# Optimization experiments

Hardware: AMD Instinct MI355X
Metric: run time of the kernel (lower is better)

The kernel has to match this reference:

```python
import jax, jax.numpy as jnp
import numpy as np

UNITS = 1024
EMBED = 512
K = 32000
HIDDEN_LAYERS = 2
BATCH = 64
SEQ = 256
ALPHA = 0.2  # leaky_relu slope


def _leaky_relu(z):
    return jnp.where(z > 0, z, ALPHA * z)


def setup_inputs() -> dict:
    key = jax.random.key(0)
    ks = jax.random.split(key, 10)
    s_in = 1.0 / np.sqrt(UNITS)
    s_e = 1.0 / np.sqrt(EMBED)
    return {
        "x": jax.random.randint(ks[0], (BATCH, SEQ), 0, K),
        "x_embedding": jax.random.normal(ks[1], (K, EMBED), dtype=jnp.float32) * 0.05,
        "w_y": jax.random.normal(ks[2], (UNITS, UNITS), dtype=jnp.float32) * s_in,
        "w_x": jax.random.normal(ks[3], (EMBED, UNITS), dtype=jnp.float32) * s_e,
        "b_in": jax.random.uniform(ks[4], (UNITS,), dtype=jnp.float32, minval=-0.05, maxval=0.05),
        "w_hidden": jax.random.normal(ks[5], (HIDDEN_LAYERS, UNITS, UNITS), dtype=jnp.float32) * s_in,
        "b_hidden": jax.random.uniform(ks[6], (HIDDEN_LAYERS, UNITS), dtype=jnp.float32, minval=-0.05, maxval=0.05),
        "w_out": jax.random.normal(ks[7], (UNITS, UNITS), dtype=jnp.float32) * s_in,
        "b_out": jax.random.uniform(ks[8], (UNITS,), dtype=jnp.float32, minval=-0.05, maxval=0.05),
        "h0": jax.random.uniform(ks[9], (1, UNITS), dtype=jnp.float32, minval=-0.05, maxval=0.05),
    }


def reference(x, x_embedding, w_y, w_x, b_in, w_hidden, b_hidden, w_out, b_out, h0):
    n = x.shape[0]
    # Gather all embeddings up front: [n, T, E] -> time-major [T, n, E]
    xe_all = jnp.swapaxes(x_embedding[x], 0, 1)

    def step(y0, xe):
        # MLPUnit: sum of input projections + bias, inner activation
        h = _leaky_relu(y0 @ w_y + xe @ w_x + b_in)

        def layer(hc, wb):
            w, bb = wb
            return _leaky_relu(hc @ w + bb), None

        h, _ = jax.lax.scan(layer, h, (w_hidden, b_hidden))
        y1 = y0 + (h @ w_out + b_out)  # highway residual
        return y1, y1

    y0 = jnp.broadcast_to(h0, (n, h0.shape[1]))
    _, yr = jax.lax.scan(step, y0, xe_all)  # [T, n, units]
    return jnp.swapaxes(yr, 0, 1)  # [n, T, units]
```

## Files before the change

### kernel.cpp

```cpp
#include <hip/hip_runtime.h>


constexpr int B = 64, T = 256, U = 1024, E = 512;
constexpr int BU = B * U;
constexpr int APITCH = 1156;
constexpr int RPITCH = 264;

#define LRELU(v) ((v) > 0.f ? (v) : 0.2f * (v))

using f4 = float __attribute__((ext_vector_type(4)));

__device__ __forceinline__ void llc_store(float* p, float v) {
  __hip_atomic_store(p, v, __ATOMIC_RELAXED, __HIP_MEMORY_SCOPE_AGENT);
}
__device__ __forceinline__ unsigned llc_flag(const unsigned* p) {
  return __hip_atomic_load(p, __ATOMIC_RELAXED, __HIP_MEMORY_SCOPE_AGENT);
}
__device__ __forceinline__ void llc_post(unsigned* p, unsigned v) {
  __hip_atomic_store(p, v, __ATOMIC_RELAXED, __HIP_MEMORY_SCOPE_AGENT);
}

__global__ void k_init(float* __restrict__ slot1, float* __restrict__ ybuf,
                       const float* __restrict__ h0,
                       unsigned* __restrict__ flags) {
  int tid = blockIdx.x * 256 + threadIdx.x;
  if (tid < 512) flags[tid] = 0u;
  if (tid < BU) {
    float v = h0[tid & (U - 1)];
    slot1[tid] = v;
    ybuf[tid] = v;
  }
}

__global__ __launch_bounds__(256) void k_xproj(
    const int* __restrict__ x, const float* __restrict__ emb,
    const float* __restrict__ w_x, const float* __restrict__ b_in,
    float* __restrict__ xp) {
  __shared__ float a_s[64][36];
  __shared__ float w_s[32][64];
  __shared__ int idxs[64];
  const int tid = threadIdx.x;
  const int m0 = blockIdx.x * 64;
  const int c0 = blockIdx.y * 64;
  if (tid < 64) {
    int m = m0 + tid;
    idxs[tid] = x[(m & 63) * T + (m >> 6)];
  }
  __syncthreads();
  const int rq = tid >> 4, cq = tid & 15;
  float acc[4][4] = {};
  for (int k0 = 0; k0 < E; k0 += 32) {
#pragma unroll
    for (int rep = 0; rep < 8; ++rep) {
      int e = rep * 256 + tid;
      int r = e >> 5, k = e & 31;
      a_s[r][k] = emb[(size_t)idxs[r] * E + k0 + k];
    }
#pragma unroll
    for (int rep = 0; rep < 2; ++rep) {
      int e = rep * 256 + tid;
      int kr = e >> 4, q = e & 15;
      *(float4*)&w_s[kr][4 * q] =
          *(const float4*)(w_x + (size_t)(k0 + kr) * U + c0 + 4 * q);
    }
    __syncthreads();
#pragma unroll
    for (int kc = 0; kc < 32; kc += 4) {
      float4 a4[4], w4[4];
#pragma unroll
      for (int i = 0; i < 4; ++i) a4[i] = *(const float4*)&a_s[4 * rq + i][kc];
#pragma unroll
      for (int kk = 0; kk < 4; ++kk)
        w4[kk] = *(const float4*)&w_s[kc + kk][4 * cq];
#pragma unroll
      for (int i = 0; i < 4; ++i) {
        const float av[4] = {a4[i].x, a4[i].y, a4[i].z, a4[i].w};
#pragma unroll
        for (int kk = 0; kk < 4; ++kk) {
          acc[i][0] += av[kk] * w4[kk].x;
          acc[i][1] += av[kk] * w4[kk].y;
          acc[i][2] += av[kk] * w4[kk].z;
          acc[i][3] += av[kk] * w4[kk].w;
        }
      }
    }
    __syncthreads();
  }
  const float4 bb = *(const float4*)(b_in + c0 + 4 * cq);
  const float bv[4] = {bb.x, bb.y, bb.z, bb.w};
#pragma unroll
  for (int i = 0; i < 4; ++i) {
    float4 o;
    o.x = acc[i][0] + bv[0];
    o.y = acc[i][1] + bv[1];
    o.z = acc[i][2] + bv[2];
    o.w = acc[i][3] + bv[3];
    *(float4*)(xp + (size_t)(m0 + 4 * rq + i) * U + c0 + 4 * cq) = o;
  }
}

__global__ __launch_bounds__(512, 2) void k_seq(
    const float* __restrict__ xp, const float* __restrict__ w_y,
    const float* __restrict__ w_h, const float* __restrict__ b_h,
    const float* __restrict__ w_out, const float* __restrict__ b_out,
    float* __restrict__ out, float* __restrict__ slots,
    float* __restrict__ ybuf, unsigned* __restrict__ flags) {
  __shared__ float a_s[8 * APITCH];
  __shared__ float red2[64 * RPITCH];
  const int tid = threadIdx.x;
  const int bid = blockIdx.x;
  const int cg = ((bid & 7) << 2) | ((bid >> 3) & 3);
  const int rg = bid >> 5;
  const int w = tid >> 6, l = tid & 63;
  const int ci = l & 7;
  const int sp = w * 8 + (l >> 3);
  const int cb = 4 * ci, k0 = 16 * sp;
  const int abase_k = 36 * (sp >> 1) + 16 * (sp & 1);
  const int frow = 8 * rg + (tid >> 5);
  const int fu = 32 * cg + (tid & 31);
  const int tb = tid >> 8;
  const int kq = ((tid & 255) + 8 * cg) & 255;
  const int lofs = 36 * (kq >> 3) + ((4 * kq) & 31);

  auto wbase = [&](int P) -> const float* {
    const int p = P & 3;
    const float* Wsrc = (p == 0)   ? w_y
                        : (p == 3) ? w_out
                                   : w_h + (size_t)(p - 1) * U * U;
    return Wsrc + (size_t)k0 * U + 32 * cg + cb;
  };
  f4 wreg[16];
  {
    const float* wp = wbase(0);
#pragma unroll
    for (int j = 0; j < 16; ++j) wreg[j] = *(const f4*)(wp + (size_t)j * U);
  }

  for (int P = 0; P < 4 * T; ++P) {
    const int t = P >> 2, p = P & 3;
    const float* Asrc =
        slots + (size_t)((P + 1) & 1) * BU + (size_t)(8 * rg) * U;
    float* slotw = slots + (size_t)(P & 1) * BU;
    if (P > 0) {
      if (tid < 64) {
        const unsigned tgt = (unsigned)P;
        const unsigned* fp = &flags[rg * 32 + (l & 31)];
        while (!__all(llc_flag(fp) >= tgt)) __builtin_amdgcn_s_sleep(1);
      }
      __syncthreads();
      asm volatile("" ::: "memory");
    }
    float preA = 0.f, preB = 0.f;
    if (tid < 256) {
      if (p == 0)
        preA = xp[((size_t)t * B + frow) * U + fu];
      else if (p < 3)
        preA = b_h[(p - 1) * U + fu];
      else {
        preA = ybuf[(size_t)frow * U + fu];
        preB = b_out[fu];
      }
    }
    {
      const float* pb = Asrc + 4 * kq;
      f4 av0, av1, av2, av3;
      asm volatile("global_load_dwordx4 %0, %1, off sc1"
                   : "=v"(av0)
                   : "v"(pb + (size_t)tb * U));
      asm volatile("global_load_dwordx4 %0, %1, off sc1"
                   : "=v"(av1)
                   : "v"(pb + (size_t)(tb + 2) * U));
      asm volatile("global_load_dwordx4 %0, %1, off sc1"
                   : "=v"(av2)
                   : "v"(pb + (size_t)(tb + 4) * U));
      asm volatile("global_load_dwordx4 %0, %1, off sc1"
                   : "=v"(av3)
                   : "v"(pb + (size_t)(tb + 6) * U));
      asm volatile("s_waitcnt vmcnt(0)" ::: "memory");
      *(f4*)&a_s[(tb + 0) * APITCH + lofs] = av0;
      *(f4*)&a_s[(tb + 2) * APITCH + lofs] = av1;
      *(f4*)&a_s[(tb + 4) * APITCH + lofs] = av2;
      *(f4*)&a_s[(tb + 6) * APITCH + lofs] = av3;
    }
    __syncthreads();
    f4 acc[8];
#pragma unroll
    for (int r = 0; r < 8; ++r) acc[r] = (f4){0.f, 0.f, 0.f, 0.f};
#pragma unroll
    for (int q = 0; q < 4; ++q) {
      const f4 w0 = wreg[4 * q], w1 = wreg[4 * q + 1];
      const f4 w2 = wreg[4 * q + 2], w3 = wreg[4 * q + 3];
      const int ab = abase_k + 4 * q;
#pragma unroll
      for (int r = 0; r < 8; ++r) {
        f4 a = *(const f4*)&a_s[r * APITCH + ab];
        acc[r] += a.x * w0 + a.y * w1 + a.z * w2 + a.w * w3;
      }
    }
#pragma unroll
    for (int r = 0; r < 8; ++r)
      *(f4*)&red2[sp * RPITCH + r * 32 + cb] = acc[r];
    __syncthreads();
    float yn = 0.f;
    bool wout = false;
    if (tid < 256) {
      float s0 = 0.f, s1 = 0.f, s2 = 0.f, s3 = 0.f;
#pragma unroll
      for (int z = 0; z < 64; z += 4) {
        s0 += red2[(z + 0) * RPITCH + tid];
        s1 += red2[(z + 1) * RPITCH + tid];
        s2 += red2[(z + 2) * RPITCH + tid];
        s3 += red2[(z + 3) * RPITCH + tid];
      }
      const float sum = (s0 + s1) + (s2 + s3);
      const size_t yi = (size_t)frow * U + fu;
      if (p < 3) {
        float v = sum + preA;
        llc_store(slotw + yi, LRELU(v));
      } else {
        yn = preA + preB + sum;
        ybuf[yi] = yn;
        llc_store(slotw + yi, yn);
        wout = true;
      }
    }
    asm volatile("" ::: "memory");
    __builtin_amdgcn_s_waitcnt(0);
    __syncthreads();
    if (tid == 0) llc_post(&flags[rg * 32 + cg], (unsigned)(P + 1));
    if (wout) out[((size_t)frow * T + t) * U + fu] = yn;
    if (P < 4 * T - 1) {
      const float* wp = wbase(P + 1);
#pragma unroll
      for (int j = 0; j < 16; ++j) wreg[j] = *(const f4*)(wp + (size_t)j * U);
    }
  }
}

extern "C" void kernel_launch(void* const* d_in, const int* in_sizes, int n_in,
                              void* d_out, int out_size, void* d_ws,
                              size_t ws_size, hipStream_t stream) {
  const int* x = (const int*)d_in[0];
  const float* emb = (const float*)d_in[1];
  const float* w_y = (const float*)d_in[2];
  const float* w_x = (const float*)d_in[3];
  const float* b_in = (const float*)d_in[4];
  const float* w_h = (const float*)d_in[5];
  const float* b_h = (const float*)d_in[6];
  const float* w_out = (const float*)d_in[7];
  const float* b_out = (const float*)d_in[8];
  const float* h0 = (const float*)d_in[9];
  float* out = (float*)d_out;

  float* ws = (float*)d_ws;
  float* xpb = ws;
  float* slots = xpb + (size_t)T * B * U;
  float* ybuf = slots + 2 * (size_t)BU;
  unsigned* flags = (unsigned*)(ybuf + (size_t)BU);

  k_init<<<256, 256, 0, stream>>>(slots + (size_t)BU, ybuf, h0, flags);
  dim3 g1(256, 16);
  k_xproj<<<g1, 256, 0, stream>>>(x, emb, w_x, b_in, xpb);

  void* args[] = {&xpb,   &w_y, &w_h,   &b_h,  &w_out,
                  &b_out, &out, &slots, &ybuf, &flags};
  hipLaunchCooperativeKernel((void*)k_seq, dim3(256), dim3(512), args, 0u,
                             stream);
}
```

Before: 5.141 ms.

## Fold w_out into w_y to remove one grid-synchronized phase per timestep

Precomputes W2 = w_out·w_y per block column slice in a prologue, so the pre-activation of the next step is u_{t+1} = u_t + h·W2 + b_out·w_y plus the x projection. This cuts the serial chain from four grid-synced matmul phases per timestep to three. The y output is computed off the critical path with the ordinary w_out matmul after the flag is posted. In exchange it adds a costly 1024-deep prologue GEMM, doubles the weight registers, and changes floating-point accumulation order.

```diff
diff --git a/kernel.cpp b/kernel.cpp
--- a/kernel.cpp
+++ b/kernel.cpp
@@ -5,6 +5,7 @@
 constexpr int BU = B * U;
 constexpr int APITCH = 1156;
 constexpr int RPITCH = 264;
+constexpr int WOPITCH = 9;
 
 #define LRELU(v) ((v) > 0.f ? (v) : 0.2f * (v))
 
@@ -20,16 +21,24 @@
   __hip_atomic_store(p, v, __ATOMIC_RELAXED, __HIP_MEMORY_SCOPE_AGENT);
 }
 
-__global__ void k_init(float* __restrict__ slot1, float* __restrict__ ybuf,
-                       const float* __restrict__ h0,
-                       unsigned* __restrict__ flags) {
+#define COMPUTE_ACC(WB)                                          \
+  do {                                                           \
+    _Pragma("unroll") for (int r = 0; r < 8; ++r) acc[r] =       \
+        (f4){0.f, 0.f, 0.f, 0.f};                                \
+    _Pragma("unroll") for (int q = 0; q < 4; ++q) {              \
+      const f4 w0 = WB[4 * q], w1 = WB[4 * q + 1];               \
+      const f4 w2 = WB[4 * q + 2], w3 = WB[4 * q + 3];           \
+      const int ab = abase_k + 4 * q;                            \
+      _Pragma("unroll") for (int r = 0; r < 8; ++r) {            \
+        f4 a = *(const f4*)&a_s[r * APITCH + ab];                \
+        acc[r] += a.x * w0 + a.y * w1 + a.z * w2 + a.w * w3;     \
+      }                                                          \
+    }                                                            \
+  } while (0)
+
+__global__ void k_init(unsigned* __restrict__ flags) {
   int tid = blockIdx.x * 256 + threadIdx.x;
   if (tid < 512) flags[tid] = 0u;
-  if (tid < BU) {
-    float v = h0[tid & (U - 1)];
-    slot1[tid] = v;
-    ybuf[tid] = v;
-  }
 }
 
 __global__ __launch_bounds__(256) void k_xproj(
@@ -103,10 +112,11 @@
     const float* __restrict__ xp, const float* __restrict__ w_y,
     const float* __restrict__ w_h, const float* __restrict__ b_h,
     const float* __restrict__ w_out, const float* __restrict__ b_out,
-    float* __restrict__ out, float* __restrict__ slots,
-    float* __restrict__ ybuf, unsigned* __restrict__ flags) {
+    const float* __restrict__ h0, float* __restrict__ out,
+    float* __restrict__ slots, unsigned* __restrict__ flags) {
   __shared__ float a_s[8 * APITCH];
   __shared__ float red2[64 * RPITCH];
+  __shared__ float c2_s[32], u0_s[32];
   const int tid = threadIdx.x;
   const int bid = blockIdx.x;
   const int cg = ((bid & 7) << 2) | ((bid >> 3) & 3);
@@ -122,42 +132,107 @@
   const int kq = ((tid & 255) + 8 * cg) & 255;
   const int lofs = 36 * (kq >> 3) + ((4 * kq) & 31);
 
-  auto wbase = [&](int P) -> const float* {
-    const int p = P & 3;
-    const float* Wsrc = (p == 0)   ? w_y
-                        : (p == 3) ? w_out
-                                   : w_h + (size_t)(p - 1) * U * U;
-    return Wsrc + (size_t)k0 * U + 32 * cg + cb;
-  };
+  float* const wos = red2;
+  float* const wys = a_s;
+  f4 w2reg[16];
+#pragma unroll
+  for (int jj = 0; jj < 16; ++jj) w2reg[jj] = (f4){0.f, 0.f, 0.f, 0.f};
+  f4 c2a = (f4){0.f, 0.f, 0.f, 0.f}, u0a = (f4){0.f, 0.f, 0.f, 0.f};
+  {
+    f4 nx0, nx1, nx2, nx3, nwy;
+    {
+      const float* wo = w_out + (size_t)tid * U;
+      nx0 = *(const f4*)wo;
+      nx1 = *(const f4*)(wo + 4);
+      const float* wo2 = w_out + (size_t)(tid + 512) * U;
+      nx2 = *(const f4*)wo2;
+      nx3 = *(const f4*)(wo2 + 4);
+      if (tid < 64)
+        nwy = *(const f4*)(w_y + (size_t)(tid >> 3) * U + 32 * cg +
+                           4 * (tid & 7));
+    }
+    for (int mi = 0; mi < 128; ++mi) {
+      const int m0 = mi * 8;
+#pragma unroll
+      for (int q = 0; q < 4; ++q) {
+        wos[tid * WOPITCH + q] = nx0[q];
+        wos[tid * WOPITCH + 4 + q] = nx1[q];
+        wos[(tid + 512) * WOPITCH + q] = nx2[q];
+        wos[(tid + 512) * WOPITCH + 4 + q] = nx3[q];
+      }
+      if (tid < 64) *(f4*)&wys[(tid >> 3) * 36 + 4 * (tid & 7)] = nwy;
+      __syncthreads();
+      if (mi < 127) {
+        const int m1 = m0 + 8;
+        const float* wo = w_out + (size_t)tid * U + m1;
+        nx0 = *(const f4*)wo;
+        nx1 = *(const f4*)(wo + 4);
+        const float* wo2 = w_out + (size_t)(tid + 512) * U + m1;
+        nx2 = *(const f4*)wo2;
+        nx3 = *(const f4*)(wo2 + 4);
+        if (tid < 64)
+          nwy = *(const f4*)(w_y + (size_t)(m1 + (tid >> 3)) * U + 32 * cg +
+                             4 * (tid & 7));
+      }
+#pragma unroll
+      for (int mm = 0; mm < 8; ++mm) {
+        const f4 wy = *(const f4*)&wys[mm * 36 + cb];
+#pragma unroll
+        for (int jj = 0; jj < 16; ++jj)
+          w2reg[jj] += wos[(16 * sp + jj) * WOPITCH + mm] * wy;
+        if (tid < 8) {
+          c2a += b_out[m0 + mm] * wy;
+          u0a += h0[m0 + mm] * wy;
+        }
+      }
+      __syncthreads();
+    }
+  }
+  if (tid < 8) {
+    *(f4*)&c2_s[cb] = c2a;
+    *(f4*)&u0_s[cb] = u0a;
+  }
+  __syncthreads();
+  float u_reg = 0.f, y_reg = 0.f, c2_lane = 0.f;
+  if (tid < 256) {
+    c2_lane = c2_s[tid & 31];
+    u_reg = u0_s[tid & 31];
+    y_reg = h0[fu];
+    float h1 = LRELU(u_reg + xp[(size_t)frow * U + fu]);
+    llc_store(slots + (size_t)frow * U + fu, h1);
+  }
+  asm volatile("" ::: "memory");
+  __builtin_amdgcn_s_waitcnt(0);
+  __syncthreads();
+  if (tid == 0) llc_post(&flags[rg * 32 + cg], 1u);
+
   f4 wreg[16];
   {
-    const float* wp = wbase(0);
-#pragma unroll
-    for (int j = 0; j < 16; ++j) wreg[j] = *(const f4*)(wp + (size_t)j * U);
-  }
-
-  for (int P = 0; P < 4 * T; ++P) {
-    const int t = P >> 2, p = P & 3;
+    const float* wp = w_h + (size_t)k0 * U + 32 * cg + cb;
+#pragma unroll
+    for (int jj = 0; jj < 16; ++jj) wreg[jj] = *(const f4*)(wp + (size_t)jj * U);
+  }
+
+  for (int Q = 1; Q <= 3 * T; ++Q) {
+    const int j = (Q - 1) % 3, t = (Q - 1) / 3;
     const float* Asrc =
-        slots + (size_t)((P + 1) & 1) * BU + (size_t)(8 * rg) * U;
-    float* slotw = slots + (size_t)(P & 1) * BU;
-    if (P > 0) {
-      if (tid < 64) {
-        const unsigned tgt = (unsigned)P;
-        const unsigned* fp = &flags[rg * 32 + (l & 31)];
-        while (!__all(llc_flag(fp) >= tgt)) __builtin_amdgcn_s_sleep(1);
-      }
-      __syncthreads();
-      asm volatile("" ::: "memory");
-    }
+        slots + (size_t)((Q + 1) & 1) * BU + (size_t)(8 * rg) * U;
+    float* slotw = slots + (size_t)(Q & 1) * BU;
+    if (tid < 64) {
+      const unsigned tgt = (unsigned)Q;
+      const unsigned* fp = &flags[rg * 32 + (l & 31)];
+      while (!__all(llc_flag(fp) >= tgt)) __builtin_amdgcn_s_sleep(1);
+    }
+    __syncthreads();
+    asm volatile("" ::: "memory");
     float preA = 0.f, preB = 0.f;
     if (tid < 256) {
-      if (p == 0)
-        preA = xp[((size_t)t * B + frow) * U + fu];
-      else if (p < 3)
-        preA = b_h[(p - 1) * U + fu];
+      if (j == 0)
+        preA = b_h[fu];
+      else if (j == 1)
+        preA = b_h[U + fu];
       else {
-        preA = ybuf[(size_t)frow * U + fu];
+        if (t < T - 1) preA = xp[((size_t)(t + 1) * B + frow) * U + fu];
         preB = b_out[fu];
       }
     }
@@ -184,25 +259,14 @@
     }
     __syncthreads();
     f4 acc[8];
-#pragma unroll
-    for (int r = 0; r < 8; ++r) acc[r] = (f4){0.f, 0.f, 0.f, 0.f};
-#pragma unroll
-    for (int q = 0; q < 4; ++q) {
-      const f4 w0 = wreg[4 * q], w1 = wreg[4 * q + 1];
-      const f4 w2 = wreg[4 * q + 2], w3 = wreg[4 * q + 3];
-      const int ab = abase_k + 4 * q;
-#pragma unroll
-      for (int r = 0; r < 8; ++r) {
-        f4 a = *(const f4*)&a_s[r * APITCH + ab];
-        acc[r] += a.x * w0 + a.y * w1 + a.z * w2 + a.w * w3;
-      }
-    }
+    if (j == 2)
+      COMPUTE_ACC(w2reg);
+    else
+      COMPUTE_ACC(wreg);
 #pragma unroll
     for (int r = 0; r < 8; ++r)
       *(f4*)&red2[sp * RPITCH + r * 32 + cb] = acc[r];
     __syncthreads();
-    float yn = 0.f;
-    bool wout = false;
     if (tid < 256) {
       float s0 = 0.f, s1 = 0.f, s2 = 0.f, s3 = 0.f;
 #pragma unroll
@@ -214,25 +278,48 @@
       }
       const float sum = (s0 + s1) + (s2 + s3);
       const size_t yi = (size_t)frow * U + fu;
-      if (p < 3) {
-        float v = sum + preA;
-        llc_store(slotw + yi, LRELU(v));
+      if (j < 2) {
+        llc_store(slotw + yi, LRELU(sum + preA));
       } else {
-        yn = preA + preB + sum;
-        ybuf[yi] = yn;
-        llc_store(slotw + yi, yn);
-        wout = true;
+        u_reg += sum + c2_lane;
+        llc_store(slotw + yi, LRELU(u_reg + preA));
       }
     }
     asm volatile("" ::: "memory");
     __builtin_amdgcn_s_waitcnt(0);
     __syncthreads();
-    if (tid == 0) llc_post(&flags[rg * 32 + cg], (unsigned)(P + 1));
-    if (wout) out[((size_t)frow * T + t) * U + fu] = yn;
-    if (P < 4 * T - 1) {
-      const float* wp = wbase(P + 1);
-#pragma unroll
-      for (int j = 0; j < 16; ++j) wreg[j] = *(const f4*)(wp + (size_t)j * U);
+    if (tid == 0) llc_post(&flags[rg * 32 + cg], (unsigned)(Q + 1));
+    if (j == 2) {
+      f4 acc2[8];
+      {
+        f4* acc = acc2;
+        if (true) COMPUTE_ACC(wreg);
+      }
+#pragma unroll
+      for (int r = 0; r < 8; ++r)
+        *(f4*)&red2[sp * RPITCH + r * 32 + cb] = acc2[r];
+      __syncthreads();
+      if (tid < 256) {
+        float s0 = 0.f, s1 = 0.f, s2 = 0.f, s3 = 0.f;
+#pragma unroll
+        for (int z = 0; z < 64; z += 4) {
+          s0 += red2[(z + 0) * RPITCH + tid];
+          s1 += red2[(z + 1) * RPITCH + tid];
+          s2 += red2[(z + 2) * RPITCH + tid];
+          s3 += red2[(z + 3) * RPITCH + tid];
+        }
+        y_reg += (s0 + s1) + (s2 + s3) + preB;
+        out[((size_t)frow * T + t) * U + fu] = y_reg;
+      }
+    }
+    if (Q < 3 * T) {
+      const float* Wn = (j == 0) ? (w_h + (size_t)U * U)
+                       : (j == 1) ? w_out
+                                  : w_h;
+      const float* wp = Wn + (size_t)k0 * U + 32 * cg + cb;
+#pragma unroll
+      for (int jj = 0; jj < 16; ++jj)
+        wreg[jj] = *(const f4*)(wp + (size_t)jj * U);
     }
   }
 }
@@ -255,15 +342,15 @@
   float* ws = (float*)d_ws;
   float* xpb = ws;
   float* slots = xpb + (size_t)T * B * U;
-  float* ybuf = slots + 2 * (size_t)BU;
-  unsigned* flags = (unsigned*)(ybuf + (size_t)BU);
-
-  k_init<<<256, 256, 0, stream>>>(slots + (size_t)BU, ybuf, h0, flags);
+  float* ybuf_dead = slots + 2 * (size_t)BU;
+  unsigned* flags = (unsigned*)(ybuf_dead + (size_t)BU);
+
+  k_init<<<2, 256, 0, stream>>>(flags);
   dim3 g1(256, 16);
   k_xproj<<<g1, 256, 0, stream>>>(x, emb, w_x, b_in, xpb);
 
-  void* args[] = {&xpb,   &w_y, &w_h,   &b_h,  &w_out,
-                  &b_out, &out, &slots, &ybuf, &flags};
+  void* args[] = {&xpb,  &w_y,   &w_h, &b_h,   &w_out,
+                  &b_out, &h0,   &out, &slots, &flags};
   hipLaunchCooperativeKernel((void*)k_seq, dim3(256), dim3(512), args, 0u,
                              stream);
 }
```

After: 4.836 ms (median of 2 runs). 5.9% less time.
